# Kernel tuning notes

Hardware: AMD Instinct MI355X
Metric: run time of the kernel (lower is better)

Reference implementation:

```python
import jax, jax.numpy as jnp
import numpy as np

B, P, E, H = 16, 1024, 1024, 16
DH = E // H  # 64


def setup_inputs() -> dict:
    key = jax.random.key(0)
    ks = jax.random.split(key, 7)
    # kaiming_uniform on [H, DH, DH]: bound = sqrt(6 / fan_in), fan_in = DH
    bound = float(np.sqrt(6.0 / DH))
    w_att_val = jax.random.uniform(ks[0], (H, DH, DH), jnp.float32, -bound, bound)
    attention_bias = jax.random.normal(ks[1], (H, P, P), jnp.float32)
    lb = float(1.0 / np.sqrt(E))
    wv_w = jax.random.uniform(ks[2], (E, E), jnp.float32, -lb, lb)
    wv_b = jax.random.uniform(ks[3], (E,), jnp.float32, -lb, lb)
    out_w = jax.random.uniform(ks[4], (E, E), jnp.float32, -lb, lb)
    out_b = jax.random.uniform(ks[5], (E,), jnp.float32, -lb, lb)
    x = jax.random.normal(ks[6], (B, P, E), jnp.float32)
    return {"x": x, "w_att_val": w_att_val, "attention_bias": attention_bias,
            "wv_w": wv_w, "wv_b": wv_b, "out_w": out_w, "out_b": out_b}


def reference(x, w_att_val, attention_bias, wv_w, wv_b, out_w, out_b):
    b, p, e = x.shape
    dh = e // H
    # split heads: [B, H, P, DH]
    x_h = x.reshape(b, p, H, dh).transpose(0, 2, 1, 3)
    # bilinear scores: (x_h @ W) @ x_h^T -> [B, H, P, P]
    xw = jnp.einsum('bhpd,hde->bhpe', x_h, w_att_val)
    scores = jnp.einsum('bhpe,bhqe->bhpq', xw, x_h)
    scores = scores / jnp.sqrt(jnp.asarray(dh, x.dtype)) + attention_bias
    attn = jax.nn.softmax(scores, axis=-1)
    # values: Linear(E, E) then split heads
    vx = x @ wv_w.T + wv_b
    vx = vx.reshape(b, p, H, dh).transpose(0, 2, 1, 3)
    out = jnp.einsum('bhpq,bhqd->bhpd', attn, vx)
    out = out.transpose(0, 2, 1, 3).reshape(b, p, e)
    return out @ out_w.T + out_b
```

## Files before the change

kernel.cpp:

```cpp
#include <hip/hip_runtime.h>

#define PB 16
#define PP 1024
#define PE 1024
#define PH 16
#define PDH 64

typedef __attribute__((ext_vector_type(8))) short bf16x8;
typedef __attribute__((ext_vector_type(4))) short bf16x4;
typedef __attribute__((ext_vector_type(4))) float f32x4;

#define LOG2E 1.44269504088896340736f

__device__ __forceinline__ short f2bf(float f) {
    union { float f; unsigned u; } a;
    a.f = f;
    unsigned u = a.u;
    u += 0x7fffu + ((u >> 16) & 1u);
    return (short)(u >> 16);
}
__device__ __forceinline__ float bf2f(short s) {
    union { unsigned u; float f; } a;
    a.u = ((unsigned)(unsigned short)s) << 16;
    return a.f;
}
__device__ __forceinline__ unsigned cvtpk(float lo, float hi) {
    unsigned r;
    asm("v_cvt_pk_bf16_f32 %0, %1, %2" : "=v"(r) : "v"(lo), "v"(hi));
    return r;
}
union U8 { unsigned u[4]; bf16x8 v; };
__device__ __forceinline__ void async16(const void* g, void* l) {
    __builtin_amdgcn_global_load_lds(
        (const __attribute__((address_space(1))) unsigned int*)g,
        (__attribute__((address_space(3))) unsigned int*)l, 16, 0, 0);
}

__global__ __launch_bounds__(256) void bias_conv(const float* __restrict__ bias,
                                                 short* __restrict__ biasb) {
    size_t idx = ((size_t)blockIdx.x * 256 + threadIdx.x) * 8;
    float4 a = *(const float4*)(bias + idx);
    float4 b = *(const float4*)(bias + idx + 4);
    bf16x8 t = {f2bf(a.x * LOG2E), f2bf(a.y * LOG2E), f2bf(a.z * LOG2E), f2bf(a.w * LOG2E),
                f2bf(b.x * LOG2E), f2bf(b.y * LOG2E), f2bf(b.z * LOG2E), f2bf(b.w * LOG2E)};
    *(bf16x8*)(biasb + idx) = t;
}

__global__ __launch_bounds__(256) void wconv(const float* __restrict__ wvw,
                                             const float* __restrict__ outw,
                                             short* __restrict__ wvwb,
                                             short* __restrict__ outwb) {
    int bid = blockIdx.x;
    const float* src = (bid < 512) ? wvw : outw;
    short* dst = (bid < 512) ? wvwb : outwb;
    int lb = (bid < 512) ? bid : bid - 512;
    size_t idx = ((size_t)lb * 256 + threadIdx.x) * 8;
    float4 a = *(const float4*)(src + idx);
    float4 b = *(const float4*)(src + idx + 4);
    bf16x8 t = {f2bf(a.x), f2bf(a.y), f2bf(a.z), f2bf(a.w),
                f2bf(b.x), f2bf(b.y), f2bf(b.z), f2bf(b.w)};
    *(bf16x8*)(dst + idx) = t;
}

__global__ __launch_bounds__(256) void xw_kernel(const float* __restrict__ x,
                                                 const float* __restrict__ watt,
                                                 short* __restrict__ xw,
                                                 short* __restrict__ xbf) {
    int bid = blockIdx.x;
    int q4 = bid & 3;
    int bh = bid >> 2;
    int h = bh & 15;
    __shared__ short Wt[64][88];

    int tid = threadIdx.x;
    {
        const float* W = watt + (size_t)h * 4096;
        int idx = tid * 16;
        int d = idx >> 6, e0 = idx & 63;
#pragma unroll
        for (int i = 0; i < 16; i += 4) {
            float4 v = *(const float4*)(W + d * 64 + e0 + i);
            Wt[e0 + i + 0][d] = f2bf(v.x);
            Wt[e0 + i + 1][d] = f2bf(v.y);
            Wt[e0 + i + 2][d] = f2bf(v.z);
            Wt[e0 + i + 3][d] = f2bf(v.w);
        }
    }
    __syncthreads();

    int wave = tid >> 6, lane = tid & 63;
    int lm = lane & 15, lq = lane >> 4;

    bf16x8 bfr[4][2];
#pragma unroll
    for (int nt = 0; nt < 4; nt++)
#pragma unroll
        for (int kf = 0; kf < 2; kf++)
            bfr[nt][kf] = *(const bf16x8*)&Wt[nt * 16 + lm][kf * 32 + lq * 8];

    int b = bh >> 4;
    const float QSCALE = 0.125f * LOG2E;
    for (int pass = 0; pass < 4; pass++) {
        int p0 = q4 * 256 + pass * 64 + wave * 16;
        const float* xrow = x + ((size_t)(b * 1024 + p0 + lm)) * 1024 + h * 64;
        short* xorow = xbf + ((size_t)(b * 1024 + p0 + lm)) * 1024 + h * 64;
        bf16x8 af[2];
#pragma unroll
        for (int kf = 0; kf < 2; kf++) {
            float4 v0 = *(const float4*)(xrow + kf * 32 + lq * 8);
            float4 v1 = *(const float4*)(xrow + kf * 32 + lq * 8 + 4);
            bf16x8 t;
            t[0] = f2bf(v0.x); t[1] = f2bf(v0.y); t[2] = f2bf(v0.z); t[3] = f2bf(v0.w);
            t[4] = f2bf(v1.x); t[5] = f2bf(v1.y); t[6] = f2bf(v1.z); t[7] = f2bf(v1.w);
            af[kf] = t;
            *(bf16x8*)(xorow + kf * 32 + lq * 8) = t;
        }
#pragma unroll
        for (int nt = 0; nt < 4; nt++) {
            f32x4 acc = {0.f, 0.f, 0.f, 0.f};
            acc = __builtin_amdgcn_mfma_f32_16x16x32_bf16(af[0], bfr[nt][0], acc, 0, 0, 0);
            acc = __builtin_amdgcn_mfma_f32_16x16x32_bf16(af[1], bfr[nt][1], acc, 0, 0, 0);
            size_t base = ((size_t)bh * 1024 + p0 + lq * 4) * 64 + nt * 16 + lm;
#pragma unroll
            for (int r = 0; r < 4; r++)
                xw[base + (size_t)r * 64] = f2bf(acc[r] * QSCALE);
        }
    }
}

__global__ __launch_bounds__(256) void vx_gemm(const short* __restrict__ xbf,
                                               const short* __restrict__ wvwb,
                                               const float* __restrict__ wvb,
                                               short* __restrict__ vt) {
    int mblk = blockIdx.x >> 3, nblk = blockIdx.x & 7;
    int m0 = mblk * 128, n0 = nblk * 128;
    __shared__ short As[128 * 32];
    __shared__ short Bs[128 * 32];

    int tid = threadIdx.x;
    int wv = tid >> 6, ln = tid & 63;
    int c0 = wv * 2;
    int rrow = ln >> 2, rseg = (ln & 3) * 8;
    const short* gA = xbf + (size_t)(m0 + c0 * 16 + rrow) * 1024 + rseg;
    const short* gB = wvwb + (size_t)(n0 + c0 * 16 + rrow) * 1024 + rseg;
    short* lA = As + c0 * 512;
    short* lB = Bs + c0 * 512;

    int lane = ln, lm = lane & 15, lq = lane >> 4;
    int wm = (wv >> 1) * 64, wn = (wv & 1) * 64;

    f32x4 acc[4][4];
#pragma unroll
    for (int i = 0; i < 4; i++)
#pragma unroll
        for (int j = 0; j < 4; j++) acc[i][j] = (f32x4){0.f, 0.f, 0.f, 0.f};

    for (int k0 = 0; k0 < 1024; k0 += 32) {
        __syncthreads();
        async16(gA + k0, lA);
        async16(gA + k0 + 16 * 1024, lA + 512);
        async16(gB + k0, lB);
        async16(gB + k0 + 16 * 1024, lB + 512);
        __syncthreads();
        bf16x8 af[4], bfr[4];
#pragma unroll
        for (int mt = 0; mt < 4; mt++) af[mt] = *(const bf16x8*)&As[(wm + mt * 16 + lm) * 32 + lq * 8];
#pragma unroll
        for (int nt = 0; nt < 4; nt++) bfr[nt] = *(const bf16x8*)&Bs[(wn + nt * 16 + lm) * 32 + lq * 8];
#pragma unroll
        for (int mt = 0; mt < 4; mt++)
#pragma unroll
            for (int nt = 0; nt < 4; nt++)
                acc[mt][nt] = __builtin_amdgcn_mfma_f32_16x16x32_bf16(af[mt], bfr[nt], acc[mt][nt], 0, 0, 0);
    }

#pragma unroll
    for (int nt = 0; nt < 4; nt++) {
        int e = n0 + wn + nt * 16 + lm;
        float bias = wvb[e];
        int hh = e >> 6, dd = e & 63;
#pragma unroll
        for (int mt = 0; mt < 4; mt++) {
            int pg = m0 + wm + mt * 16 + lq * 4;
            int bb = pg >> 10, pp = pg & 1023;
            bf16x4 pk;
#pragma unroll
            for (int r = 0; r < 4; r++) pk[r] = f2bf(acc[mt][nt][r] + bias);
            *(bf16x4*)(vt + ((size_t)((bb * 16 + hh) * 64 + dd)) * 1024 + pp) = pk;
        }
    }
}

__global__ __launch_bounds__(256, 3) void flash_kernel(const short* __restrict__ xbf,
                                                       const short* __restrict__ xw,
                                                       const short* __restrict__ vt,
                                                       const short* __restrict__ biasb,
                                                       short* __restrict__ obuf) {
    int bid = blockIdx.x;
    int qblk = bid & 7, b = (bid >> 3) & 15, h = bid >> 7;
    int bh = b * 16 + h;
    int q0 = qblk * 128;

    __shared__ short Ks[64][72];
    __shared__ short Vs[64][72];
    __shared__ float Rs[4][36];

    int tid = threadIdx.x, wave = tid >> 6, lane = tid & 63;
    int lm = lane & 15, lq = lane >> 4;

    bf16x8 qa[2][2];
#pragma unroll
    for (int qt = 0; qt < 2; qt++)
#pragma unroll
        for (int kf = 0; kf < 2; kf++)
            qa[qt][kf] = *(const bf16x8*)(xw + ((size_t)bh * 1024 + q0 + wave * 32 + qt * 16 + lm) * 64 + kf * 32 + lq * 8);

    f32x4 o[2][4];
#pragma unroll
    for (int qt = 0; qt < 2; qt++)
#pragma unroll
        for (int dt = 0; dt < 4; dt++) o[qt][dt] = (f32x4){0.f, 0.f, 0.f, 0.f};
    float rs[2] = {0.f, 0.f};

    int ci0 = tid * 2, ci1 = tid * 2 + 1;
    int r0 = ci0 >> 3, s0 = (ci0 & 7) * 8;
    int r1 = ci1 >> 3, s1 = (ci1 & 7) * 8;
    const short* kg = xbf + ((size_t)(b * 1024)) * 1024 + h * 64;
    const short* vg = vt + ((size_t)bh * 64) * 1024;
    const short* bg = biasb + ((size_t)h << 20) + (size_t)(q0 + wave * 32) * 1024;

    bf16x8 kr[2], vr[2];
    bf16x4 br[4][2];
    kr[0] = *(const bf16x8*)(kg + (size_t)r0 * 1024 + s0);
    kr[1] = *(const bf16x8*)(kg + (size_t)r1 * 1024 + s1);
    vr[0] = *(const bf16x8*)(vg + (size_t)r0 * 1024 + s0);
    vr[1] = *(const bf16x8*)(vg + (size_t)r1 * 1024 + s1);
#pragma unroll
    for (int kt = 0; kt < 4; kt++)
#pragma unroll
        for (int qt = 0; qt < 2; qt++)
            br[kt][qt] = *(const bf16x4*)(bg + (size_t)(qt * 16 + lm) * 1024 + kt * 16 + lq * 4);
    *(bf16x8*)&Ks[r0][s0] = kr[0];
    *(bf16x8*)&Ks[r1][s1] = kr[1];
    *(bf16x8*)&Vs[r0][s0] = vr[0];
    *(bf16x8*)&Vs[r1][s1] = vr[1];

    for (int tile = 0; tile < 16; tile++) {
        int kv0 = tile * 64;
        __syncthreads();

        f32x4 s[4][2];
#pragma unroll
        for (int kt = 0; kt < 4; kt++)
#pragma unroll
            for (int qt = 0; qt < 2; qt++) {
                bf16x4 bv = br[kt][qt];
                s[kt][qt] = (f32x4){bf2f(bv[0]), bf2f(bv[1]), bf2f(bv[2]), bf2f(bv[3])};
            }

        if (tile < 15) {
            int kvn = kv0 + 64;
            kr[0] = *(const bf16x8*)(kg + (size_t)(kvn + r0) * 1024 + s0);
            kr[1] = *(const bf16x8*)(kg + (size_t)(kvn + r1) * 1024 + s1);
            vr[0] = *(const bf16x8*)(vg + (size_t)r0 * 1024 + kvn + s0);
            vr[1] = *(const bf16x8*)(vg + (size_t)r1 * 1024 + kvn + s1);
#pragma unroll
            for (int kt = 0; kt < 4; kt++)
#pragma unroll
                for (int qt = 0; qt < 2; qt++)
                    br[kt][qt] = *(const bf16x4*)(bg + (size_t)(qt * 16 + lm) * 1024 + kvn + kt * 16 + lq * 4);
        }

#pragma unroll
        for (int kf = 0; kf < 2; kf++) {
            bf16x8 ka[4];
#pragma unroll
            for (int kt = 0; kt < 4; kt++)
                ka[kt] = *(const bf16x8*)&Ks[kt * 16 + lm][kf * 32 + lq * 8];
#pragma unroll
            for (int kt = 0; kt < 4; kt++)
#pragma unroll
                for (int qt = 0; qt < 2; qt++)
                    s[kt][qt] = __builtin_amdgcn_mfma_f32_16x16x32_bf16(ka[kt], qa[qt][kf], s[kt][qt], 0, 0, 0);
        }

#pragma unroll
        for (int kt = 0; kt < 4; kt++)
#pragma unroll
            for (int qt = 0; qt < 2; qt++)
#pragma unroll
                for (int r = 0; r < 4; r++) {
                    float pv = __builtin_amdgcn_exp2f(s[kt][qt][r]);
                    s[kt][qt][r] = pv;
                    rs[qt] += pv;
                }

#pragma unroll
        for (int kf = 0; kf < 2; kf++) {
            bf16x8 pa[2];
#pragma unroll
            for (int qt = 0; qt < 2; qt++) {
                U8 u;
                u.u[0] = cvtpk(s[kf * 2][qt][0], s[kf * 2][qt][1]);
                u.u[1] = cvtpk(s[kf * 2][qt][2], s[kf * 2][qt][3]);
                u.u[2] = cvtpk(s[kf * 2 + 1][qt][0], s[kf * 2 + 1][qt][1]);
                u.u[3] = cvtpk(s[kf * 2 + 1][qt][2], s[kf * 2 + 1][qt][3]);
                pa[qt] = u.v;
            }
#pragma unroll
            for (int dt = 0; dt < 4; dt++) {
                U8 uv;
                *(bf16x4*)&uv.u[0] = *(const bf16x4*)&Vs[dt * 16 + lm][kf * 32 + lq * 4];
                *(bf16x4*)&uv.u[2] = *(const bf16x4*)&Vs[dt * 16 + lm][kf * 32 + 16 + lq * 4];
#pragma unroll
                for (int qt = 0; qt < 2; qt++)
                    o[qt][dt] = __builtin_amdgcn_mfma_f32_16x16x32_bf16(pa[qt], uv.v, o[qt][dt], 0, 0, 0);
            }
        }

        __syncthreads();
        if (tile < 15) {
            *(bf16x8*)&Ks[r0][s0] = kr[0];
            *(bf16x8*)&Ks[r1][s1] = kr[1];
            *(bf16x8*)&Vs[r0][s0] = vr[0];
            *(bf16x8*)&Vs[r1][s1] = vr[1];
        }
    }

#pragma unroll
    for (int qt = 0; qt < 2; qt++) {
        rs[qt] += __shfl_xor(rs[qt], 16);
        rs[qt] += __shfl_xor(rs[qt], 32);
    }
    if (lq == 0) { Rs[wave][lm] = rs[0]; Rs[wave][16 + lm] = rs[1]; }
    __syncthreads();

#pragma unroll
    for (int qt = 0; qt < 2; qt++) {
        float inv[4];
#pragma unroll
        for (int r = 0; r < 4; r++)
            inv[r] = 1.f / Rs[wave][qt * 16 + lq * 4 + r];
#pragma unroll
        for (int dt = 0; dt < 4; dt++) {
            int e = h * 64 + dt * 16 + lm;
#pragma unroll
            for (int r = 0; r < 4; r++) {
                int p = q0 + wave * 32 + qt * 16 + lq * 4 + r;
                obuf[((size_t)(b * 1024 + p)) * 1024 + e] = f2bf(o[qt][dt][r] * inv[r]);
            }
        }
    }
}

__global__ __launch_bounds__(256) void out_gemm(const short* __restrict__ obuf,
                                                const short* __restrict__ outwb,
                                                const float* __restrict__ outb,
                                                float* __restrict__ out) {
    int mblk = blockIdx.x >> 3, nblk = blockIdx.x & 7;
    int m0 = mblk * 128, n0 = nblk * 128;
    __shared__ short As[128 * 32];
    __shared__ short Bs[128 * 32];

    int tid = threadIdx.x;
    int wv = tid >> 6, ln = tid & 63;
    int c0 = wv * 2;
    int rrow = ln >> 2, rseg = (ln & 3) * 8;
    const short* gA = obuf + (size_t)(m0 + c0 * 16 + rrow) * 1024 + rseg;
    const short* gB = outwb + (size_t)(n0 + c0 * 16 + rrow) * 1024 + rseg;
    short* lA = As + c0 * 512;
    short* lB = Bs + c0 * 512;

    int lm = ln & 15, lq = ln >> 4;
    int wm = (wv >> 1) * 64, wn = (wv & 1) * 64;

    f32x4 acc[4][4];
#pragma unroll
    for (int i = 0; i < 4; i++)
#pragma unroll
        for (int j = 0; j < 4; j++) acc[i][j] = (f32x4){0.f, 0.f, 0.f, 0.f};

    for (int k0 = 0; k0 < 1024; k0 += 32) {
        __syncthreads();
        async16(gA + k0, lA);
        async16(gA + k0 + 16 * 1024, lA + 512);
        async16(gB + k0, lB);
        async16(gB + k0 + 16 * 1024, lB + 512);
        __syncthreads();
        bf16x8 af[4], bfr[4];
#pragma unroll
        for (int mt = 0; mt < 4; mt++) af[mt] = *(const bf16x8*)&As[(wm + mt * 16 + lm) * 32 + lq * 8];
#pragma unroll
        for (int nt = 0; nt < 4; nt++) bfr[nt] = *(const bf16x8*)&Bs[(wn + nt * 16 + lm) * 32 + lq * 8];
#pragma unroll
        for (int mt = 0; mt < 4; mt++)
#pragma unroll
            for (int nt = 0; nt < 4; nt++)
                acc[mt][nt] = __builtin_amdgcn_mfma_f32_16x16x32_bf16(af[mt], bfr[nt], acc[mt][nt], 0, 0, 0);
    }

#pragma unroll
    for (int nt = 0; nt < 4; nt++) {
        int e = n0 + wn + nt * 16 + lm;
        float bias = outb[e];
#pragma unroll
        for (int mt = 0; mt < 4; mt++) {
            int pg = m0 + wm + mt * 16 + lq * 4;
#pragma unroll
            for (int r = 0; r < 4; r++)
                out[(size_t)(pg + r) * 1024 + e] = acc[mt][nt][r] + bias;
        }
    }
}

extern "C" void kernel_launch(void* const* d_in, const int* in_sizes, int n_in,
                              void* d_out, int out_size, void* d_ws, size_t ws_size,
                              hipStream_t stream) {
    const float* x    = (const float*)d_in[0];
    const float* watt = (const float*)d_in[1];
    const float* bias = (const float*)d_in[2];
    const float* wvw  = (const float*)d_in[3];
    const float* wvb  = (const float*)d_in[4];
    const float* outw = (const float*)d_in[5];
    const float* outb = (const float*)d_in[6];
    float* out = (float*)d_out;

    char* ws = (char*)d_ws;
    short* xw     = (short*)ws;
    short* vt     = (short*)(ws + ((size_t)32 << 20));
    short* obuf   = (short*)(ws + ((size_t)64 << 20));
    short* biasb  = (short*)(ws + ((size_t)96 << 20));
    short* xbf    = (short*)(ws + ((size_t)128 << 20));
    short* wvwb   = (short*)(ws + ((size_t)160 << 20));
    short* outwb  = (short*)(ws + ((size_t)162 << 20));

    xw_kernel<<<PB * PH * 4, 256, 0, stream>>>(x, watt, xw, xbf);
    bias_conv<<<8192, 256, 0, stream>>>(bias, biasb);
    wconv<<<1024, 256, 0, stream>>>(wvw, outw, wvwb, outwb);
    vx_gemm<<<(PB * PP / 128) * (PE / 128), 256, 0, stream>>>(xbf, wvwb, wvb, vt);
    flash_kernel<<<PB * PH * (PP / 128), 256, 0, stream>>>(xbf, xw, vt, biasb, obuf);
    out_gemm<<<(PB * PP / 128) * (PE / 128), 256, 0, stream>>>(obuf, outwb, outb, out);
}
```

Before: 449.8 us.

## Fuse bias conversion into flash kernel, remap block order, add MFMA priority hints

Removes the separate bias_conv pass. The flash kernel now reads the fp32 attention bias directly and scales it by log2e inline, which saves a 64MB read plus a 32MB write in a standalone kernel. In exchange, each flash block reads the bias in fp32 (twice the bytes of bf16), and those reads repeat across the 16 batches. It also remaps block indices in vx_gemm, out_gemm and the flash kernel so that blocks sharing data are spread across the XCDs, and wraps the MFMA sections in s_setprio to favour matrix issue.

```diff
diff --git a/kernel.cpp b/kernel.cpp
--- a/kernel.cpp
+++ b/kernel.cpp
@@ -34,16 +34,6 @@
     __builtin_amdgcn_global_load_lds(
         (const __attribute__((address_space(1))) unsigned int*)g,
         (__attribute__((address_space(3))) unsigned int*)l, 16, 0, 0);
-}
-
-__global__ __launch_bounds__(256) void bias_conv(const float* __restrict__ bias,
-                                                 short* __restrict__ biasb) {
-    size_t idx = ((size_t)blockIdx.x * 256 + threadIdx.x) * 8;
-    float4 a = *(const float4*)(bias + idx);
-    float4 b = *(const float4*)(bias + idx + 4);
-    bf16x8 t = {f2bf(a.x * LOG2E), f2bf(a.y * LOG2E), f2bf(a.z * LOG2E), f2bf(a.w * LOG2E),
-                f2bf(b.x * LOG2E), f2bf(b.y * LOG2E), f2bf(b.z * LOG2E), f2bf(b.w * LOG2E)};
-    *(bf16x8*)(biasb + idx) = t;
 }
 
 __global__ __launch_bounds__(256) void wconv(const float* __restrict__ wvw,
@@ -132,7 +122,8 @@
                                                const short* __restrict__ wvwb,
                                                const float* __restrict__ wvb,
                                                short* __restrict__ vt) {
-    int mblk = blockIdx.x >> 3, nblk = blockIdx.x & 7;
+    int logical = (blockIdx.x & 7) * 128 + (blockIdx.x >> 3);
+    int mblk = logical >> 3, nblk = logical & 7;
     int m0 = mblk * 128, n0 = nblk * 128;
     __shared__ short As[128 * 32];
     __shared__ short Bs[128 * 32];
@@ -194,10 +185,10 @@
 __global__ __launch_bounds__(256, 3) void flash_kernel(const short* __restrict__ xbf,
                                                        const short* __restrict__ xw,
                                                        const short* __restrict__ vt,
-                                                       const short* __restrict__ biasb,
+                                                       const float* __restrict__ bias,
                                                        short* __restrict__ obuf) {
-    int bid = blockIdx.x;
-    int qblk = bid & 7, b = (bid >> 3) & 15, h = bid >> 7;
+    int logical = (blockIdx.x & 7) * 256 + (blockIdx.x >> 3);
+    int qblk = logical & 7, b = (logical >> 3) & 15, h = logical >> 7;
     int bh = b * 16 + h;
     int q0 = qblk * 128;
 
@@ -227,10 +218,10 @@
     int r1 = ci1 >> 3, s1 = (ci1 & 7) * 8;
     const short* kg = xbf + ((size_t)(b * 1024)) * 1024 + h * 64;
     const short* vg = vt + ((size_t)bh * 64) * 1024;
-    const short* bg = biasb + ((size_t)h << 20) + (size_t)(q0 + wave * 32) * 1024;
+    const float* bg = bias + ((size_t)h << 20) + (size_t)(q0 + wave * 32) * 1024;
 
     bf16x8 kr[2], vr[2];
-    bf16x4 br[4][2];
+    float4 br[4][2];
     kr[0] = *(const bf16x8*)(kg + (size_t)r0 * 1024 + s0);
     kr[1] = *(const bf16x8*)(kg + (size_t)r1 * 1024 + s1);
     vr[0] = *(const bf16x8*)(vg + (size_t)r0 * 1024 + s0);
@@ -239,7 +230,7 @@
     for (int kt = 0; kt < 4; kt++)
 #pragma unroll
         for (int qt = 0; qt < 2; qt++)
-            br[kt][qt] = *(const bf16x4*)(bg + (size_t)(qt * 16 + lm) * 1024 + kt * 16 + lq * 4);
+            br[kt][qt] = *(const float4*)(bg + (size_t)(qt * 16 + lm) * 1024 + kt * 16 + lq * 4);
     *(bf16x8*)&Ks[r0][s0] = kr[0];
     *(bf16x8*)&Ks[r1][s1] = kr[1];
     *(bf16x8*)&Vs[r0][s0] = vr[0];
@@ -254,8 +245,8 @@
         for (int kt = 0; kt < 4; kt++)
 #pragma unroll
             for (int qt = 0; qt < 2; qt++) {
-                bf16x4 bv = br[kt][qt];
-                s[kt][qt] = (f32x4){bf2f(bv[0]), bf2f(bv[1]), bf2f(bv[2]), bf2f(bv[3])};
+                float4 bv = br[kt][qt];
+                s[kt][qt] = (f32x4){bv.x * LOG2E, bv.y * LOG2E, bv.z * LOG2E, bv.w * LOG2E};
             }
 
         if (tile < 15) {
@@ -268,9 +259,10 @@
             for (int kt = 0; kt < 4; kt++)
 #pragma unroll
                 for (int qt = 0; qt < 2; qt++)
-                    br[kt][qt] = *(const bf16x4*)(bg + (size_t)(qt * 16 + lm) * 1024 + kvn + kt * 16 + lq * 4);
-        }
-
+                    br[kt][qt] = *(const float4*)(bg + (size_t)(qt * 16 + lm) * 1024 + kvn + kt * 16 + lq * 4);
+        }
+
+        __builtin_amdgcn_s_setprio(1);
 #pragma unroll
         for (int kf = 0; kf < 2; kf++) {
             bf16x8 ka[4];
@@ -283,6 +275,7 @@
                 for (int qt = 0; qt < 2; qt++)
                     s[kt][qt] = __builtin_amdgcn_mfma_f32_16x16x32_bf16(ka[kt], qa[qt][kf], s[kt][qt], 0, 0, 0);
         }
+        __builtin_amdgcn_s_setprio(0);
 
 #pragma unroll
         for (int kt = 0; kt < 4; kt++)
@@ -295,6 +288,7 @@
                     rs[qt] += pv;
                 }
 
+        __builtin_amdgcn_s_setprio(1);
 #pragma unroll
         for (int kf = 0; kf < 2; kf++) {
             bf16x8 pa[2];
@@ -317,6 +311,7 @@
                     o[qt][dt] = __builtin_amdgcn_mfma_f32_16x16x32_bf16(pa[qt], uv.v, o[qt][dt], 0, 0, 0);
             }
         }
+        __builtin_amdgcn_s_setprio(0);
 
         __syncthreads();
         if (tile < 15) {
@@ -357,7 +352,8 @@
                                                 const short* __restrict__ outwb,
                                                 const float* __restrict__ outb,
                                                 float* __restrict__ out) {
-    int mblk = blockIdx.x >> 3, nblk = blockIdx.x & 7;
+    int logical = (blockIdx.x & 7) * 128 + (blockIdx.x >> 3);
+    int mblk = logical >> 3, nblk = logical & 7;
     int m0 = mblk * 128, n0 = nblk * 128;
     __shared__ short As[128 * 32];
     __shared__ short Bs[128 * 32];
@@ -429,15 +425,13 @@
     short* xw     = (short*)ws;
     short* vt     = (short*)(ws + ((size_t)32 << 20));
     short* obuf   = (short*)(ws + ((size_t)64 << 20));
-    short* biasb  = (short*)(ws + ((size_t)96 << 20));
-    short* xbf    = (short*)(ws + ((size_t)128 << 20));
-    short* wvwb   = (short*)(ws + ((size_t)160 << 20));
-    short* outwb  = (short*)(ws + ((size_t)162 << 20));
+    short* xbf    = (short*)(ws + ((size_t)96 << 20));
+    short* wvwb   = (short*)(ws + ((size_t)128 << 20));
+    short* outwb  = (short*)(ws + ((size_t)130 << 20));
 
     xw_kernel<<<PB * PH * 4, 256, 0, stream>>>(x, watt, xw, xbf);
-    bias_conv<<<8192, 256, 0, stream>>>(bias, biasb);
     wconv<<<1024, 256, 0, stream>>>(wvw, outw, wvwb, outwb);
     vx_gemm<<<(PB * PP / 128) * (PE / 128), 256, 0, stream>>>(xbf, wvwb, wvb, vt);
-    flash_kernel<<<PB * PH * (PP / 128), 256, 0, stream>>>(xbf, xw, vt, biasb, obuf);
+    flash_kernel<<<PB * PH * (PP / 128), 256, 0, stream>>>(xbf, xw, vt, bias, obuf);
     out_gemm<<<(PB * PP / 128) * (PE / 128), 256, 0, stream>>>(obuf, outwb, outb, out);
 }
```

New measurement: 423.2 us. 5.9% less time.
